# Kernel optimization log

Measured on AMD Instinct MI355X. Metric: run time of the kernel, lower is better.

Reference implementation:

```python
import jax, jax.numpy as jnp
import numpy as np

BS, NUM_VISIT, MAX_FEAT, MAX_TARGET = 32, 6, 12, 16
NUM_FEAT, NUM_REL, HIDDEN, REDUCED, OUT = 1992, 11, 128, 256, 90
GAMMA = 0.1


def setup_inputs() -> dict:
    key = jax.random.key(0)
    ks = jax.random.split(key, 20)
    u = lambda k, shape: jax.random.uniform(k, shape, dtype=jnp.float32)
    # one/multi-hot-like dense float inputs (per docstring)
    feat_index = (u(ks[0], (BS, NUM_VISIT, MAX_FEAT, NUM_FEAT)) < 0.01).astype(jnp.float32)
    neighbor_index = (u(ks[1], (BS, NUM_VISIT, MAX_FEAT, MAX_TARGET, NUM_FEAT)) < 0.001).astype(jnp.float32)
    rel_index = (u(ks[2], (BS, NUM_VISIT, MAX_FEAT, MAX_TARGET, NUM_REL)) < 0.2).astype(jnp.float32)
    # parameters (torch.rand init in the original; xavier for embedding)
    bound = float(np.sqrt(6.0 / (NUM_FEAT + HIDDEN)))
    emb_weight = jax.random.uniform(ks[3], (NUM_FEAT, HIDDEN), dtype=jnp.float32, minval=-bound, maxval=bound)
    return {
        "feat_index": feat_index,
        "neighbor_index": neighbor_index,
        "rel_index": rel_index,
        "emb_weight": emb_weight,
        "W_edge": u(ks[4], (NUM_REL, HIDDEN)),
        "W_v": u(ks[5], (REDUCED, HIDDEN)),
        "W_r": u(ks[6], (REDUCED, HIDDEN)),
        "b_v": u(ks[7], (REDUCED,)),
        "b_r": u(ks[8], (REDUCED,)),
        "W_alpha": u(ks[9], (NUM_FEAT,)),
        "b_alpha": u(ks[10], (MAX_FEAT,)),
        "W_beta": u(ks[11], (MAX_FEAT,)),
        "b_beta": u(ks[12], (NUM_VISIT,)),
        "W_l": u(ks[13], (REDUCED, REDUCED)),
        "b_l": u(ks[14], (REDUCED,)),
        "fc_W": u(ks[15], (OUT, 2 * REDUCED)) * 0.05,
        "fc_b": u(ks[16], (OUT,)) * 0.05,
    }


def reference(feat_index, neighbor_index, rel_index, emb_weight, W_edge, W_v, W_r,
              b_v, b_r, W_alpha, b_alpha, W_beta, b_beta, W_l, b_l, fc_W, fc_b):
    num_visit = feat_index.shape[1]
    # decay buffer lamb[i] = exp(-gamma*(num_visit - i))
    lamb = jnp.exp(-GAMMA * (num_visit - jnp.arange(num_visit, dtype=feat_index.dtype)))

    # node-level attention alpha: (b,v,m)
    alpha = jax.nn.softmax(jnp.einsum('n,bvmn->bvm', W_alpha, feat_index) + b_alpha)
    # visit-level attention beta: (b,v), modulated by temporal decay
    beta = jnp.tanh(jnp.einsum('m,bvm->bv', W_beta, alpha) + b_beta) * lamb

    # reduced node embeddings: (num_feat, reduced)
    reduced_emb = emb_weight @ W_v.T + b_v
    # attention-weighted neighbor aggregation; sum over targets t fused in
    attn = alpha * beta[:, :, None]                       # (b,v,m)
    node_agg = jnp.einsum('bvm,bvmtn,nr->bvmr', attn, neighbor_index, reduced_emb)

    # reduced edge (relation) embeddings: (num_rel, reduced)
    reduced_edge = W_edge @ W_r.T + b_r
    edge_agg = jnp.einsum('bvmtr,rd->bvmd', rel_index, reduced_edge)  # sum over t fused

    agg = node_agg + edge_agg                             # (b,v,m,reduced)
    # einsum('dd, bvfd -> bvfd') in torch takes the diagonal of W_l
    h = jax.nn.relu(jnp.diagonal(W_l) * agg + b_l)        # (b,v,m,reduced)

    h_g = h.sum(axis=(1, 2))                              # (b, reduced)
    # einsum('bvmn,bvmr->bvnr').sum(n).sum(v) == contract over v,m,n
    h_p = jnp.einsum('bvm,bvmr->br', feat_index.sum(-1), h)

    z_joint = jnp.concatenate([h_g, h_p], axis=-1)        # (b, 2*reduced)
    return jax.nn.sigmoid(z_joint @ fc_W.T + fc_b)
```

## Files before the change

### kernel.cpp

```cpp
#include <hip/hip_runtime.h>
#include <math.h>

#define BS   32
#define NV   6
#define MF   12
#define MT   16
#define NF   1992
#define NR   11
#define HID  128
#define RED  256
#define OUTD 90
#define GAMMA 0.1f

#define WS_HG    0
#define WS_HP    (WS_HG + BS*RED)
#define WS_ATTN  (WS_HP + BS*RED)
#define WS_FSUM  (WS_ATTN + BS*NV*MF)
#define WS_REMB  (WS_FSUM + BS*NV*MF)
#define WS_REDGE (WS_REMB + NF*RED)

__global__ void k_reduce_emb(const float* __restrict__ emb, const float* __restrict__ W_edge,
                             const float* __restrict__ W_v, const float* __restrict__ W_r,
                             const float* __restrict__ b_v, const float* __restrict__ b_r,
                             float* __restrict__ remb, float* __restrict__ redge) {
    __shared__ float row[HID];
    int blk = blockIdx.x;
    int tid = threadIdx.x;
    const float *src, *W, *bias;
    float* dst;
    if (blk < NF) { src = emb + (size_t)blk * HID;        W = W_v; bias = b_v; dst = remb  + (size_t)blk * RED; }
    else          { src = W_edge + (size_t)(blk-NF) * HID; W = W_r; bias = b_r; dst = redge + (size_t)(blk-NF) * RED; }
    if (tid < HID) row[tid] = src[tid];
    __syncthreads();
    const float* wrow = W + (size_t)tid * HID;
    float acc = bias[tid];
    #pragma unroll 4
    for (int k = 0; k < HID; ++k) acc += row[k] * wrow[k];
    dst[tid] = acc;
}

__global__ void k_attn(const float* __restrict__ feat, const float* __restrict__ W_alpha,
                       const float* __restrict__ b_alpha, const float* __restrict__ W_beta,
                       const float* __restrict__ b_beta,
                       float* __restrict__ attn_ws, float* __restrict__ fsum_ws) {
    int bv  = blockIdx.x;
    int v   = bv % NV;
    int tid = threadIdx.x;
    __shared__ float red_a[256], red_b[256];
    __shared__ float dot12[MF], fs12[MF];
    const float* base = feat + (size_t)bv * MF * NF;
    for (int m = 0; m < MF; ++m) {
        const float* rw = base + (size_t)m * NF;
        float da = 0.f, fs = 0.f;
        for (int n = tid; n < NF; n += 256) {
            float x = rw[n];
            da += W_alpha[n] * x;
            fs += x;
        }
        red_a[tid] = da; red_b[tid] = fs;
        __syncthreads();
        for (int s = 128; s > 0; s >>= 1) {
            if (tid < s) { red_a[tid] += red_a[tid+s]; red_b[tid] += red_b[tid+s]; }
            __syncthreads();
        }
        if (tid == 0) { dot12[m] = red_a[0]; fs12[m] = red_b[0]; }
        __syncthreads();
    }
    if (tid == 0) {
        float logits[MF];
        float mx = -1e30f;
        for (int m = 0; m < MF; ++m) { logits[m] = dot12[m] + b_alpha[m]; mx = fmaxf(mx, logits[m]); }
        float s = 0.f;
        for (int m = 0; m < MF; ++m) { logits[m] = expf(logits[m] - mx); s += logits[m]; }
        float inv = 1.f / s;
        float bdot = 0.f;
        for (int m = 0; m < MF; ++m) { logits[m] *= inv; bdot += W_beta[m] * logits[m]; }
        float lamb = expf(-GAMMA * (float)(NV - v));
        float beta = tanhf(bdot + b_beta[v]) * lamb;
        for (int m = 0; m < MF; ++m) {
            attn_ws[bv*MF + m] = logits[m] * beta;
            fsum_ws[bv*MF + m] = fs12[m];
        }
    }
}

#define NZCAP 1024
__global__ __launch_bounds__(256) void k_agg(
        const float* __restrict__ nbr, const float* __restrict__ rel,
        const float* __restrict__ remb, const float* __restrict__ redge,
        const float* __restrict__ attn_ws, const float* __restrict__ fsum_ws,
        const float* __restrict__ W_l, const float* __restrict__ b_l,
        float* __restrict__ h_g, float* __restrict__ h_p) {
    int bvm = blockIdx.x;
    int b   = bvm / (NV * MF);
    int tid = threadIdx.x;
    __shared__ __align__(16) float nsum[NF];
    __shared__ int   nz_n[NZCAP];
    __shared__ float nz_v[NZCAP];
    __shared__ float rsum[NR];
    __shared__ int   cnt;
    if (tid == 0) cnt = 0;

    const float4* base = (const float4*)(nbr + (size_t)bvm * MT * NF);
    float4 a0 = make_float4(0.f, 0.f, 0.f, 0.f);
    float4 a1 = make_float4(0.f, 0.f, 0.f, 0.f);
    const bool has1 = (tid + 256) < 498;
    #pragma unroll 4
    for (int t = 0; t < MT; ++t) {
        const float4* r4 = base + t * 498;
        float4 x = r4[tid];
        a0.x += x.x; a0.y += x.y; a0.z += x.z; a0.w += x.w;
        if (has1) {
            float4 y = r4[tid + 256];
            a1.x += y.x; a1.y += y.y; a1.z += y.z; a1.w += y.w;
        }
    }
    ((float4*)nsum)[tid] = a0;
    if (has1) ((float4*)nsum)[tid + 256] = a1;

    if (tid < NR) {
        const float* rb = rel + (size_t)bvm * MT * NR;
        float s = 0.f;
        #pragma unroll
        for (int t = 0; t < MT; ++t) s += rb[t*NR + tid];
        rsum[tid] = s;
    }
    __syncthreads();

    {
        float vals0[4] = {a0.x, a0.y, a0.z, a0.w};
        int nb = tid * 4;
        #pragma unroll
        for (int c = 0; c < 4; ++c) {
            if (vals0[c] != 0.f) {
                int p = atomicAdd(&cnt, 1);
                if (p < NZCAP) { nz_n[p] = nb + c; nz_v[p] = vals0[c]; }
            }
        }
        if (has1) {
            float vals1[4] = {a1.x, a1.y, a1.z, a1.w};
            nb = (tid + 256) * 4;
            #pragma unroll
            for (int c = 0; c < 4; ++c) {
                if (vals1[c] != 0.f) {
                    int p = atomicAdd(&cnt, 1);
                    if (p < NZCAP) { nz_n[p] = nb + c; nz_v[p] = vals1[c]; }
                }
            }
        }
    }
    __syncthreads();

    int r = tid;
    int c = min(cnt, NZCAP);
    float node = 0.f;
    for (int i = 0; i < c; ++i)
        node += nz_v[i] * remb[(size_t)nz_n[i] * RED + r];
    float edge = 0.f;
    #pragma unroll
    for (int j = 0; j < NR; ++j)
        edge += rsum[j] * redge[j*RED + r];
    float a  = attn_ws[bvm];
    float fs = fsum_ws[bvm];
    float agg = a * node + edge;
    float h = fmaxf(0.f, W_l[(size_t)r * RED + r] * agg + b_l[r]);
    atomicAdd(&h_g[b*RED + r], h);
    atomicAdd(&h_p[b*RED + r], fs * h);
}

__global__ void k_out(const float* __restrict__ h_g, const float* __restrict__ h_p,
                      const float* __restrict__ fc_W, const float* __restrict__ fc_b,
                      float* __restrict__ out) {
    int b   = blockIdx.x;
    int tid = threadIdx.x;
    __shared__ float z[2*RED];
    for (int j = tid; j < RED; j += 128) {
        z[j]       = h_g[b*RED + j];
        z[RED + j] = h_p[b*RED + j];
    }
    __syncthreads();
    if (tid < OUTD) {
        const float* w = fc_W + (size_t)tid * (2*RED);
        float acc = fc_b[tid];
        for (int j = 0; j < 2*RED; ++j) acc += z[j] * w[j];
        out[b*OUTD + tid] = 1.f / (1.f + expf(-acc));
    }
}

extern "C" void kernel_launch(void* const* d_in, const int* in_sizes, int n_in,
                              void* d_out, int out_size, void* d_ws, size_t ws_size,
                              hipStream_t stream) {
    const float* feat    = (const float*)d_in[0];
    const float* nbr     = (const float*)d_in[1];
    const float* rel     = (const float*)d_in[2];
    const float* emb     = (const float*)d_in[3];
    const float* W_edge  = (const float*)d_in[4];
    const float* W_v     = (const float*)d_in[5];
    const float* W_r     = (const float*)d_in[6];
    const float* b_v     = (const float*)d_in[7];
    const float* b_r     = (const float*)d_in[8];
    const float* W_alpha = (const float*)d_in[9];
    const float* b_alpha = (const float*)d_in[10];
    const float* W_beta  = (const float*)d_in[11];
    const float* b_beta  = (const float*)d_in[12];
    const float* W_l     = (const float*)d_in[13];
    const float* b_l     = (const float*)d_in[14];
    const float* fc_W    = (const float*)d_in[15];
    const float* fc_b    = (const float*)d_in[16];

    float* ws    = (float*)d_ws;
    float* hg    = ws + WS_HG;
    float* hp    = ws + WS_HP;
    float* attn  = ws + WS_ATTN;
    float* fsum  = ws + WS_FSUM;
    float* remb  = ws + WS_REMB;
    float* redge = ws + WS_REDGE;

    hipMemsetAsync(hg, 0, (size_t)2 * BS * RED * sizeof(float), stream);

    k_reduce_emb<<<NF + NR, 256, 0, stream>>>(emb, W_edge, W_v, W_r, b_v, b_r, remb, redge);
    k_attn<<<BS * NV, 256, 0, stream>>>(feat, W_alpha, b_alpha, W_beta, b_beta, attn, fsum);
    k_agg<<<BS * NV * MF, 256, 0, stream>>>(nbr, rel, remb, redge, attn, fsum, W_l, b_l, hg, hp);
    k_out<<<BS, 128, 0, stream>>>(hg, hp, fc_W, fc_b, (float*)d_out);
}
```

Measured before the change: 541.2 us.

## Transpose weights for coalesced access, batch embedding rows, and use wave-level attention reductions

Adds a prep kernel that transposes W_v, W_r and fc_W into workspace, so the embedding reduction and output GEMV read weights coalesced across threads. The embedding kernel now handles four rows per block to reuse each weight load. The attention pass is fused into the same launch and uses float4 loads with per-wave shuffle reductions instead of a shared-memory tree. It also drops the unused shared nsum buffer in k_agg, which lowers shared memory use. The cost is extra transpose work on every call and more workspace.

```diff
diff --git a/kernel.cpp b/kernel.cpp
--- a/kernel.cpp
+++ b/kernel.cpp
@@ -18,54 +18,66 @@
 #define WS_FSUM  (WS_ATTN + BS*NV*MF)
 #define WS_REMB  (WS_FSUM + BS*NV*MF)
 #define WS_REDGE (WS_REMB + NF*RED)
-
-__global__ void k_reduce_emb(const float* __restrict__ emb, const float* __restrict__ W_edge,
-                             const float* __restrict__ W_v, const float* __restrict__ W_r,
-                             const float* __restrict__ b_v, const float* __restrict__ b_r,
-                             float* __restrict__ remb, float* __restrict__ redge) {
-    __shared__ float row[HID];
+#define WS_WTV   (WS_REDGE + NR*RED)
+#define WS_WTR   (WS_WTV + HID*RED)
+#define WS_FCWT  (WS_WTR + HID*RED)
+
+#define N_WTV  (HID*RED)
+#define N_WTR  (HID*RED)
+#define N_FCWT (2*RED*OUTD)
+#define PREP_ELEMS (N_WTV + N_WTR + N_FCWT)
+#define PREP_BLOCKS ((PREP_ELEMS + 255) / 256)
+
+__global__ __launch_bounds__(256) void k_prep_attn(
+        const float* __restrict__ W_v, const float* __restrict__ W_r,
+        const float* __restrict__ fc_W,
+        const float* __restrict__ feat, const float* __restrict__ W_alpha,
+        const float* __restrict__ b_alpha, const float* __restrict__ W_beta,
+        const float* __restrict__ b_beta,
+        float* __restrict__ WT_v, float* __restrict__ WT_r, float* __restrict__ fcWT,
+        float* __restrict__ attn_ws, float* __restrict__ fsum_ws) {
     int blk = blockIdx.x;
     int tid = threadIdx.x;
-    const float *src, *W, *bias;
-    float* dst;
-    if (blk < NF) { src = emb + (size_t)blk * HID;        W = W_v; bias = b_v; dst = remb  + (size_t)blk * RED; }
-    else          { src = W_edge + (size_t)(blk-NF) * HID; W = W_r; bias = b_r; dst = redge + (size_t)(blk-NF) * RED; }
-    if (tid < HID) row[tid] = src[tid];
-    __syncthreads();
-    const float* wrow = W + (size_t)tid * HID;
-    float acc = bias[tid];
-    #pragma unroll 4
-    for (int k = 0; k < HID; ++k) acc += row[k] * wrow[k];
-    dst[tid] = acc;
-}
-
-__global__ void k_attn(const float* __restrict__ feat, const float* __restrict__ W_alpha,
-                       const float* __restrict__ b_alpha, const float* __restrict__ W_beta,
-                       const float* __restrict__ b_beta,
-                       float* __restrict__ attn_ws, float* __restrict__ fsum_ws) {
-    int bv  = blockIdx.x;
-    int v   = bv % NV;
-    int tid = threadIdx.x;
-    __shared__ float red_a[256], red_b[256];
+    if (blk < PREP_BLOCKS) {
+        int i = blk * 256 + tid;
+        if (i < N_WTV) {
+            int k = i >> 8, r = i & 255;
+            WT_v[i] = W_v[r * HID + k];
+        } else if (i < N_WTV + N_WTR) {
+            int j = i - N_WTV;
+            int k = j >> 8, r = j & 255;
+            WT_r[j] = W_r[r * HID + k];
+        } else if (i < PREP_ELEMS) {
+            int j = i - (N_WTV + N_WTR);
+            int jj = j / OUTD, o = j - jj * OUTD;
+            fcWT[j] = fc_W[o * (2 * RED) + jj];
+        }
+        return;
+    }
+    int bv   = blk - PREP_BLOCKS;
+    int v    = bv % NV;
+    int wave = tid >> 6;
+    int lane = tid & 63;
     __shared__ float dot12[MF], fs12[MF];
     const float* base = feat + (size_t)bv * MF * NF;
-    for (int m = 0; m < MF; ++m) {
-        const float* rw = base + (size_t)m * NF;
+    for (int m = wave; m < MF; m += 4) {
+        const float4* rw = (const float4*)(base + (size_t)m * NF);
+        const float4* wa = (const float4*)W_alpha;
         float da = 0.f, fs = 0.f;
-        for (int n = tid; n < NF; n += 256) {
-            float x = rw[n];
-            da += W_alpha[n] * x;
-            fs += x;
-        }
-        red_a[tid] = da; red_b[tid] = fs;
-        __syncthreads();
-        for (int s = 128; s > 0; s >>= 1) {
-            if (tid < s) { red_a[tid] += red_a[tid+s]; red_b[tid] += red_b[tid+s]; }
-            __syncthreads();
-        }
-        if (tid == 0) { dot12[m] = red_a[0]; fs12[m] = red_b[0]; }
-        __syncthreads();
-    }
+        for (int i = lane; i < NF / 4; i += 64) {
+            float4 x = rw[i];
+            float4 w = wa[i];
+            da += w.x * x.x + w.y * x.y + w.z * x.z + w.w * x.w;
+            fs += x.x + x.y + x.z + x.w;
+        }
+        #pragma unroll
+        for (int off = 32; off > 0; off >>= 1) {
+            da += __shfl_xor(da, off);
+            fs += __shfl_xor(fs, off);
+        }
+        if (lane == 0) { dot12[m] = da; fs12[m] = fs; }
+    }
+    __syncthreads();
     if (tid == 0) {
         float logits[MF];
         float mx = -1e30f;
@@ -78,9 +90,51 @@
         float lamb = expf(-GAMMA * (float)(NV - v));
         float beta = tanhf(bdot + b_beta[v]) * lamb;
         for (int m = 0; m < MF; ++m) {
-            attn_ws[bv*MF + m] = logits[m] * beta;
-            fsum_ws[bv*MF + m] = fs12[m];
-        }
+            attn_ws[bv * MF + m] = logits[m] * beta;
+            fsum_ws[bv * MF + m] = fs12[m];
+        }
+    }
+}
+
+#define NPB 4
+#define NODE_BLOCKS (NF / NPB)
+__global__ __launch_bounds__(256) void k_reduce(
+        const float* __restrict__ emb, const float* __restrict__ W_edge,
+        const float* __restrict__ WT_v, const float* __restrict__ WT_r,
+        const float* __restrict__ b_v, const float* __restrict__ b_r,
+        float* __restrict__ remb, float* __restrict__ redge) {
+    int blk = blockIdx.x;
+    int tid = threadIdx.x;
+    if (blk < NODE_BLOCKS) {
+        __shared__ float rows[NPB][HID];
+        int n0 = blk * NPB;
+        for (int i = tid; i < NPB * HID; i += 256)
+            rows[i >> 7][i & 127] = emb[(size_t)n0 * HID + i];
+        __syncthreads();
+        float bv0 = b_v[tid];
+        float a0 = bv0, a1 = bv0, a2 = bv0, a3 = bv0;
+        #pragma unroll 4
+        for (int k = 0; k < HID; ++k) {
+            float w = WT_v[k * RED + tid];
+            a0 += rows[0][k] * w;
+            a1 += rows[1][k] * w;
+            a2 += rows[2][k] * w;
+            a3 += rows[3][k] * w;
+        }
+        remb[(size_t)(n0 + 0) * RED + tid] = a0;
+        remb[(size_t)(n0 + 1) * RED + tid] = a1;
+        remb[(size_t)(n0 + 2) * RED + tid] = a2;
+        remb[(size_t)(n0 + 3) * RED + tid] = a3;
+    } else {
+        int e = blk - NODE_BLOCKS;
+        __shared__ float row[HID];
+        if (tid < HID) row[tid] = W_edge[e * HID + tid];
+        __syncthreads();
+        float acc = b_r[tid];
+        #pragma unroll 4
+        for (int k = 0; k < HID; ++k)
+            acc += row[k] * WT_r[k * RED + tid];
+        redge[e * RED + tid] = acc;
     }
 }
 
@@ -94,7 +148,6 @@
     int bvm = blockIdx.x;
     int b   = bvm / (NV * MF);
     int tid = threadIdx.x;
-    __shared__ __align__(16) float nsum[NF];
     __shared__ int   nz_n[NZCAP];
     __shared__ float nz_v[NZCAP];
     __shared__ float rsum[NR];
@@ -104,10 +157,10 @@
     const float4* base = (const float4*)(nbr + (size_t)bvm * MT * NF);
     float4 a0 = make_float4(0.f, 0.f, 0.f, 0.f);
     float4 a1 = make_float4(0.f, 0.f, 0.f, 0.f);
-    const bool has1 = (tid + 256) < 498;
+    const bool has1 = (tid + 256) < (NF / 4);
     #pragma unroll 4
     for (int t = 0; t < MT; ++t) {
-        const float4* r4 = base + t * 498;
+        const float4* r4 = base + t * (NF / 4);
         float4 x = r4[tid];
         a0.x += x.x; a0.y += x.y; a0.z += x.z; a0.w += x.w;
         if (has1) {
@@ -115,14 +168,12 @@
             a1.x += y.x; a1.y += y.y; a1.z += y.z; a1.w += y.w;
         }
     }
-    ((float4*)nsum)[tid] = a0;
-    if (has1) ((float4*)nsum)[tid + 256] = a1;
 
     if (tid < NR) {
         const float* rb = rel + (size_t)bvm * MT * NR;
         float s = 0.f;
         #pragma unroll
-        for (int t = 0; t < MT; ++t) s += rb[t*NR + tid];
+        for (int t = 0; t < MT; ++t) s += rb[t * NR + tid];
         rsum[tid] = s;
     }
     __syncthreads();
@@ -131,22 +182,20 @@
         float vals0[4] = {a0.x, a0.y, a0.z, a0.w};
         int nb = tid * 4;
         #pragma unroll
-        for (int c = 0; c < 4; ++c) {
+        for (int c = 0; c < 4; ++c)
             if (vals0[c] != 0.f) {
                 int p = atomicAdd(&cnt, 1);
                 if (p < NZCAP) { nz_n[p] = nb + c; nz_v[p] = vals0[c]; }
             }
-        }
         if (has1) {
             float vals1[4] = {a1.x, a1.y, a1.z, a1.w};
             nb = (tid + 256) * 4;
             #pragma unroll
-            for (int c = 0; c < 4; ++c) {
+            for (int c = 0; c < 4; ++c)
                 if (vals1[c] != 0.f) {
                     int p = atomicAdd(&cnt, 1);
                     if (p < NZCAP) { nz_n[p] = nb + c; nz_v[p] = vals1[c]; }
                 }
-            }
         }
     }
     __syncthreads();
@@ -159,31 +208,32 @@
     float edge = 0.f;
     #pragma unroll
     for (int j = 0; j < NR; ++j)
-        edge += rsum[j] * redge[j*RED + r];
+        edge += rsum[j] * redge[j * RED + r];
     float a  = attn_ws[bvm];
     float fs = fsum_ws[bvm];
     float agg = a * node + edge;
     float h = fmaxf(0.f, W_l[(size_t)r * RED + r] * agg + b_l[r]);
-    atomicAdd(&h_g[b*RED + r], h);
-    atomicAdd(&h_p[b*RED + r], fs * h);
+    atomicAdd(&h_g[b * RED + r], h);
+    atomicAdd(&h_p[b * RED + r], fs * h);
 }
 
 __global__ void k_out(const float* __restrict__ h_g, const float* __restrict__ h_p,
-                      const float* __restrict__ fc_W, const float* __restrict__ fc_b,
+                      const float* __restrict__ fcWT, const float* __restrict__ fc_b,
                       float* __restrict__ out) {
     int b   = blockIdx.x;
     int tid = threadIdx.x;
-    __shared__ float z[2*RED];
+    __shared__ float z[2 * RED];
     for (int j = tid; j < RED; j += 128) {
-        z[j]       = h_g[b*RED + j];
-        z[RED + j] = h_p[b*RED + j];
+        z[j]       = h_g[b * RED + j];
+        z[RED + j] = h_p[b * RED + j];
     }
     __syncthreads();
     if (tid < OUTD) {
-        const float* w = fc_W + (size_t)tid * (2*RED);
         float acc = fc_b[tid];
-        for (int j = 0; j < 2*RED; ++j) acc += z[j] * w[j];
-        out[b*OUTD + tid] = 1.f / (1.f + expf(-acc));
+        #pragma unroll 4
+        for (int j = 0; j < 2 * RED; ++j)
+            acc += z[j] * fcWT[j * OUTD + tid];
+        out[b * OUTD + tid] = 1.f / (1.f + expf(-acc));
     }
 }
 
@@ -205,8 +255,8 @@
     const float* b_beta  = (const float*)d_in[12];
     const float* W_l     = (const float*)d_in[13];
     const float* b_l     = (const float*)d_in[14];
+    const float* fc_b    = (const float*)d_in[16];
     const float* fc_W    = (const float*)d_in[15];
-    const float* fc_b    = (const float*)d_in[16];
 
     float* ws    = (float*)d_ws;
     float* hg    = ws + WS_HG;
@@ -215,11 +265,18 @@
     float* fsum  = ws + WS_FSUM;
     float* remb  = ws + WS_REMB;
     float* redge = ws + WS_REDGE;
+    float* WT_v  = ws + WS_WTV;
+    float* WT_r  = ws + WS_WTR;
+    float* fcWT  = ws + WS_FCWT;
 
     hipMemsetAsync(hg, 0, (size_t)2 * BS * RED * sizeof(float), stream);
 
-    k_reduce_emb<<<NF + NR, 256, 0, stream>>>(emb, W_edge, W_v, W_r, b_v, b_r, remb, redge);
-    k_attn<<<BS * NV, 256, 0, stream>>>(feat, W_alpha, b_alpha, W_beta, b_beta, attn, fsum);
-    k_agg<<<BS * NV * MF, 256, 0, stream>>>(nbr, rel, remb, redge, attn, fsum, W_l, b_l, hg, hp);
-    k_out<<<BS, 128, 0, stream>>>(hg, hp, fc_W, fc_b, (float*)d_out);
-}
+    k_prep_attn<<<PREP_BLOCKS + BS * NV, 256, 0, stream>>>(
+        W_v, W_r, fc_W, feat, W_alpha, b_alpha, W_beta, b_beta,
+        WT_v, WT_r, fcWT, attn, fsum);
+    k_reduce<<<NODE_BLOCKS + NR, 256, 0, stream>>>(
+        emb, W_edge, WT_v, WT_r, b_v, b_r, remb, redge);
+    k_agg<<<BS * NV * MF, 256, 0, stream>>>(
+        nbr, rel, remb, redge, attn, fsum, W_l, b_l, hg, hp);
+    k_out<<<BS, 128, 0, stream>>>(hg, hp, fcWT, fc_b, (float*)d_out);
+}
```

Result: faster. 516.9 us (-4.5%).
